# Kernel optimization log

Hardware: AMD Instinct MI355X
Metric: run time of the kernel (lower is better)

Reference implementation:

```python
import jax, jax.numpy as jnp
import numpy as np

B, S = 1, 2048
D = 2048            # n_embd
H = 16              # num heads
KV = 4              # num kv heads
GROUPS = H // KV
D_NOPE = 128
D_ROPE = 64
D_QK = D_NOPE + D_ROPE   # 192
D_V = 128
Q_RANK = 1536
KV_RANK = 512
EPS = 1e-6
MAX_POS = 4096


def rms_norm(x, w, eps=EPS):
    x32 = x.astype(jnp.float32)
    y = x32 * jax.lax.rsqrt(jnp.mean(x32 * x32, axis=-1, keepdims=True) + eps)
    return y.astype(x.dtype) * w


def rotate_half(x):
    x1, x2 = jnp.split(x, 2, axis=-1)
    return jnp.concatenate((-x2, x1), axis=-1)


def setup_inputs() -> dict:
    key = jax.random.key(0)
    ks = jax.random.split(key, 10)
    inv_freq = 1.0 / (10000.0 ** (jnp.arange(0, D_ROPE, 2, dtype=jnp.float32) / D_ROPE))
    t = jnp.arange(MAX_POS, dtype=jnp.float32)
    freqs = jnp.outer(t, inv_freq)                      # [MAX_POS, D_ROPE//2]
    emb = jnp.concatenate((freqs, freqs), axis=-1)      # [MAX_POS, D_ROPE]
    def lin(k, fan_in, fan_out):
        return jax.random.normal(k, (fan_in, fan_out), dtype=jnp.float32) * (fan_in ** -0.5)
    return {
        "hidden_states": jax.random.normal(ks[0], (B, S, D), dtype=jnp.float32),
        "cos": jnp.cos(emb)[None],                      # [1, MAX_POS, D_ROPE]
        "sin": jnp.sin(emb)[None],
        "wq_a": lin(ks[1], D, Q_RANK),
        "q_a_ln_w": jnp.ones((Q_RANK,), jnp.float32),
        "wq_b": lin(ks[2], Q_RANK, H * D_QK),
        "wkv_a": lin(ks[3], D, KV_RANK + D_ROPE),
        "kv_a_ln_w": jnp.ones((KV_RANK,), jnp.float32),
        "wkv_b": lin(ks[4], KV_RANK, KV * (D_NOPE + D_V)),
        "wo": lin(ks[5], H * D_V, D),
        "cache_position": jnp.arange(S, dtype=jnp.int64),
    }


def reference(hidden_states, cos, sin, wq_a, q_a_ln_w, wq_b, wkv_a, kv_a_ln_w,
              wkv_b, wo, cache_position):
    b, s, _ = hidden_states.shape
    # --- query low-rank path ---
    q_a = hidden_states @ wq_a                           # [B,S,Q_RANK]
    q = rms_norm(q_a, q_a_ln_w) @ wq_b                   # [B,S,H*D_QK]
    q = q.reshape(b, s, H, D_QK).transpose(0, 2, 1, 3)   # [B,H,S,D_QK]
    q_pass, q_rot = q[..., :D_NOPE], q[..., D_NOPE:]
    # --- kv low-rank path ---
    ckv = hidden_states @ wkv_a                          # [B,S,KV_RANK+D_ROPE]
    k_pass_a, k_rot_a = ckv[..., :KV_RANK], ckv[..., KV_RANK:]
    kv = rms_norm(k_pass_a, kv_a_ln_w) @ wkv_b           # [B,S,KV*(D_NOPE+D_V)]
    kv = kv.reshape(b, s, KV, D_NOPE + D_V).transpose(0, 2, 1, 3)  # [B,KV,S,*]
    k_pass, v = kv[..., :D_NOPE], kv[..., D_NOPE:]
    # --- partial RoPE ---
    c = cos[0][cache_position][None, None]               # [1,1,S,D_ROPE]
    sn = sin[0][cache_position][None, None]
    q_rot = q_rot * c + rotate_half(q_rot) * sn          # [B,H,S,D_ROPE]
    k_rot = k_rot_a[:, None]                             # [B,1,S,D_ROPE]
    k_rot = k_rot * c + rotate_half(k_rot) * sn
    k_rot = jnp.broadcast_to(k_rot, (b, KV, s, D_ROPE))
    k = jnp.concatenate((k_pass, k_rot), axis=-1)        # [B,KV,S,D_QK]
    # GQA expansion (repeat_interleave over head dim)
    k = jnp.repeat(k, GROUPS, axis=1)                    # [B,H,S,D_QK]
    v = jnp.repeat(v, GROUPS, axis=1)                    # [B,H,S,D_V]
    q_full = jnp.concatenate((q_pass, q_rot), axis=-1)   # [B,H,S,D_QK]
    # causal SDPA (default scale = 1/sqrt(D_QK), matching torch sdpa)
    scale = 1.0 / jnp.sqrt(jnp.float32(D_QK))
    scores = jnp.einsum("bhqd,bhkd->bhqk", q_full, k) * scale
    causal = jnp.tril(jnp.ones((s, s), dtype=bool))
    scores = jnp.where(causal[None, None], scores, jnp.finfo(scores.dtype).min)
    attn = jax.nn.softmax(scores, axis=-1)
    out = jnp.einsum("bhqk,bhkd->bhqd", attn, v)         # [B,H,S,D_V]
    out = out.transpose(0, 2, 1, 3).reshape(b, s, H * D_V)
    return out @ wo                                      # [B,S,D]
```

## Files before the change

### kernel.cpp

```cpp
#include <hip/hip_runtime.h>
#include <hip/hip_bf16.h>


#define S_LEN 2048
#define D_MODEL 2048
#define NH 16
#define NKV 4
#define D_QK 192
#define D_NOPE 128
#define D_ROPE 64
#define D_V 128
#define Q_RANK 1536
#define KV_RANK 512
#define CKV_PITCH 640
#define QDIM (NH * D_QK)
#define KVDIM (NKV * (D_NOPE + D_V))
#define ODIM (NH * D_V)
#define SCALE_QK 0.07216878364870322f
#define SPLIT 4

#define DT_B16 0
#define DT_F32 1
#define DT_AUTO 2

typedef __bf16 bf16x8 __attribute__((ext_vector_type(8)));
typedef float  f32x4  __attribute__((ext_vector_type(4)));
typedef unsigned short u16x8 __attribute__((ext_vector_type(8)));

typedef __attribute__((address_space(1))) const unsigned int as1_u32;
typedef __attribute__((address_space(3))) unsigned int as3_u32;

__device__ __forceinline__ void gl2lds16(const unsigned short* g, unsigned short* l) {
    __builtin_amdgcn_global_load_lds((as1_u32*)g, (as3_u32*)l, 16, 0, 0);
}

__device__ __forceinline__ float b2f(unsigned short u) {
    return __uint_as_float(((unsigned int)u) << 16);
}
__device__ __forceinline__ unsigned short f2b(float f) {
    unsigned int u = __float_as_uint(f);
    return (unsigned short)((u + 0x7fffu + ((u >> 16) & 1u)) >> 16);
}
__device__ __forceinline__ bool flag_f32(const unsigned* dt) {
    return dt[0] == 0x3F800000u;
}
__device__ __forceinline__ bool eff_f32(int mode, bool f32) {
    return mode == DT_F32 || (mode == DT_AUTO && f32);
}
__device__ __forceinline__ float ldany(const void* p, size_t i, bool f32) {
    return f32 ? ((const float*)p)[i] : b2f(((const unsigned short*)p)[i]);
}

#if __has_builtin(__builtin_amdgcn_mov_dpp)
#define ROR16F(x, n) __int_as_float(__builtin_amdgcn_mov_dpp(__float_as_int(x), 0x120 + (n), 0xf, 0xf, true))
#else
#define ROR16F(x, n) __shfl_xor((x), (n))
#endif

__global__ void __launch_bounds__(256)
cvt_bf16(const void* __restrict__ src, unsigned short* __restrict__ dst,
         int nelem, const unsigned* __restrict__ dt)
{
    const bool f32 = flag_f32(dt);
    for (int i = blockIdx.x * 256 + threadIdx.x; i < nelem; i += gridDim.x * 256)
        dst[i] = f2b(ldany(src, i, f32));
}

__global__ void __launch_bounds__(256)
transpose_w(const void* __restrict__ W, int Kdim, int Ncols,
            unsigned short* __restrict__ WT, const unsigned* __restrict__ dt)
{
    __shared__ unsigned short tile[64][65];
    const bool f32 = flag_f32(dt);
    const int k0 = blockIdx.x * 64, n0 = blockIdx.y * 64;
    const int t = threadIdx.x;

    for (int i = t; i < 4096; i += 256) {
        int r = i >> 6, c = i & 63;
        float v = (n0 + c < Ncols) ? ldany(W, (size_t)(k0 + r) * Ncols + n0 + c, f32) : 0.f;
        tile[c][r] = f2b(v);
    }
    __syncthreads();
    for (int i = t; i < 4096; i += 256) {
        int nn = i >> 6, kk = i & 63;
        WT[(size_t)(n0 + nn) * Kdim + k0 + kk] = tile[nn][kk];
    }
}

__global__ void __launch_bounds__(256)
gemm_mfma(const unsigned short* __restrict__ A, int lda,
          const unsigned short* __restrict__ BT, int ldb,
          void* __restrict__ C, int ldc, int K, int cm,
          const unsigned* __restrict__ dt,
          void* __restrict__ C2, int ldc2, int ncol1)
{
    __shared__ unsigned short As[2][128 * 32];
    __shared__ unsigned short Bs[2][128 * 32];

    const int t = threadIdx.x;
    const int w = t >> 6, lane = t & 63;
    const int wr = w & 1, wc = w >> 1;
    const int n = lane & 15, quad = lane >> 4;
    const int row0 = blockIdx.y << 7;
    int col0 = blockIdx.x << 7;
    const int e0 = (w * 64 + lane) * 8;
    const int e1 = e0 + 2048;

    f32x4 acc[4][4];
#pragma unroll
    for (int i = 0; i < 4; ++i)
#pragma unroll
        for (int j = 0; j < 4; ++j) acc[i][j] = (f32x4){0.f, 0.f, 0.f, 0.f};

    gl2lds16(A  + (size_t)(row0 + (e0 >> 5)) * lda + (e0 & 31), &As[0][e0]);
    gl2lds16(A  + (size_t)(row0 + (e1 >> 5)) * lda + (e1 & 31), &As[0][e1]);
    gl2lds16(BT + (size_t)(col0 + (e0 >> 5)) * ldb + (e0 & 31), &Bs[0][e0]);
    gl2lds16(BT + (size_t)(col0 + (e1 >> 5)) * ldb + (e1 & 31), &Bs[0][e1]);

    int cur = 0;
    for (int k0 = 0; k0 < K; k0 += 32) {
        __syncthreads();

        if (k0 + 32 < K) {
            const int kn = k0 + 32;
            gl2lds16(A  + (size_t)(row0 + (e0 >> 5)) * lda + kn + (e0 & 31), &As[cur ^ 1][e0]);
            gl2lds16(A  + (size_t)(row0 + (e1 >> 5)) * lda + kn + (e1 & 31), &As[cur ^ 1][e1]);
            gl2lds16(BT + (size_t)(col0 + (e0 >> 5)) * ldb + kn + (e0 & 31), &Bs[cur ^ 1][e0]);
            gl2lds16(BT + (size_t)(col0 + (e1 >> 5)) * ldb + kn + (e1 & 31), &Bs[cur ^ 1][e1]);
        }

        bf16x8 af[4], bfr[4];
#pragma unroll
        for (int i = 0; i < 4; ++i)
            af[i] = *(const bf16x8*)&As[cur][(wr * 64 + i * 16 + n) * 32 + quad * 8];
#pragma unroll
        for (int j = 0; j < 4; ++j)
            bfr[j] = *(const bf16x8*)&Bs[cur][(wc * 64 + j * 16 + n) * 32 + quad * 8];
#pragma unroll
        for (int i = 0; i < 4; ++i)
#pragma unroll
            for (int j = 0; j < 4; ++j)
                acc[i][j] = __builtin_amdgcn_mfma_f32_16x16x32_bf16(af[i], bfr[j], acc[i][j], 0, 0, 0);

        cur ^= 1;
    }

    void* Cp = C; int ld = ldc;
    if (col0 >= ncol1) { Cp = C2; ld = ldc2; col0 -= ncol1; }

    const bool cf = eff_f32(cm, flag_f32(dt));
#pragma unroll
    for (int i = 0; i < 4; ++i)
#pragma unroll
        for (int r = 0; r < 4; ++r) {
            const int row = row0 + wr * 64 + i * 16 + quad * 4 + r;
            if (cf) {
                float* crow = (float*)Cp + (size_t)row * ld + col0 + wc * 64 + n;
#pragma unroll
                for (int j = 0; j < 4; ++j) crow[j * 16] = acc[i][j][r];
            } else {
                unsigned short* crow = (unsigned short*)Cp + (size_t)row * ld + col0 + wc * 64 + n;
#pragma unroll
                for (int j = 0; j < 4; ++j) crow[j * 16] = f2b(acc[i][j][r]);
            }
        }
}

__global__ void __launch_bounds__(256)
rmsnorm_b(unsigned short* __restrict__ buf, int pitch, int ncols,
          const void* __restrict__ w, const unsigned* __restrict__ dt)
{
    const bool f32 = flag_f32(dt);
    const int row = blockIdx.x;
    const int t = threadIdx.x;
    unsigned short* x = buf + (size_t)row * pitch;

    float ss = 0.f;
    for (int i = t; i < ncols; i += 256) { float v = b2f(x[i]); ss += v * v; }
#pragma unroll
    for (int o = 32; o > 0; o >>= 1) ss += __shfl_down(ss, o);

    __shared__ float part[4];
    __shared__ float sc;
    if ((t & 63) == 0) part[t >> 6] = ss;
    __syncthreads();
    if (t == 0) {
        float tot = part[0] + part[1] + part[2] + part[3];
        sc = rsqrtf(tot / (float)ncols + 1e-6f);
    }
    __syncthreads();
    float scale = sc;
    for (int i = t; i < ncols; i += 256)
        x[i] = f2b(b2f(x[i]) * scale * ldany(w, i, f32));
}

__global__ void __launch_bounds__(256)
rope_k(unsigned short* __restrict__ q, unsigned short* __restrict__ ckvb,
       const void* __restrict__ cosb, const void* __restrict__ sinb,
       const void* __restrict__ cpos, const unsigned* __restrict__ dt)
{
    const bool f32 = flag_f32(dt);
    const int s = blockIdx.x;
    const int t = threadIdx.x;
    const long long* p64 = (const long long*)cpos;
    const int* p32 = (const int*)cpos;
    const bool is64 = (p64[1] == 1LL);
    const int pos = is64 ? (int)p64[s] : p32[s];
    const size_t cb = (size_t)pos * D_ROPE;

    for (int idx = t; idx < NH * 32; idx += 256) {
        int h = idx >> 5, i = idx & 31;
        unsigned short* base = q + (size_t)s * QDIM + h * D_QK + D_NOPE;
        float x1 = b2f(base[i]), x2 = b2f(base[i + 32]);
        float c1 = ldany(cosb, cb + i, f32),      s1 = ldany(sinb, cb + i, f32);
        float c2 = ldany(cosb, cb + i + 32, f32), s2 = ldany(sinb, cb + i + 32, f32);
        base[i]      = f2b(x1 * c1 - x2 * s1);
        base[i + 32] = f2b(x2 * c2 + x1 * s2);
    }
    if (t < 32) {
        int i = t;
        unsigned short* base = ckvb + (size_t)s * CKV_PITCH + KV_RANK;
        float x1 = b2f(base[i]), x2 = b2f(base[i + 32]);
        float c1 = ldany(cosb, cb + i, f32),      s1 = ldany(sinb, cb + i, f32);
        float c2 = ldany(cosb, cb + i + 32, f32), s2 = ldany(sinb, cb + i + 32, f32);
        base[i]      = f2b(x1 * c1 - x2 * s1);
        base[i + 32] = f2b(x2 * c2 + x1 * s2);
    }
}

__global__ void __launch_bounds__(256)
transpose_v(const unsigned short* __restrict__ kvb, unsigned short* __restrict__ vt)
{
    __shared__ unsigned short tile[64][68];
    const int kb = blockIdx.x;
    const int kvh = blockIdx.y >> 1;
    const int d0 = (blockIdx.y & 1) * 64;
    const int t = threadIdx.x;

    for (int i = t; i < 64 * 16; i += 256) {
        int r = i >> 4, c4 = (i & 15) << 2;
        ushort4 v = *(const ushort4*)(kvb + (size_t)(kb * 64 + r) * KVDIM
                                      + kvh * 256 + D_NOPE + d0 + c4);
        tile[c4 + 0][r] = v.x;
        tile[c4 + 1][r] = v.y;
        tile[c4 + 2][r] = v.z;
        tile[c4 + 3][r] = v.w;
    }
    __syncthreads();
    for (int i = t; i < 64 * 16; i += 256) {
        int d = i >> 4, k4 = (i & 15) << 2;
        ushort4 v = *(const ushort4*)&tile[d][k4];
        *(ushort4*)(vt + (size_t)(kvh * 128 + d0 + d) * S_LEN + kb * 64 + k4) = v;
    }
}

__global__ void __launch_bounds__(256, 2)
attn_mfma(const unsigned short* __restrict__ q, const unsigned short* __restrict__ kvb,
          const unsigned short* __restrict__ ckvb, const unsigned short* __restrict__ vt,
          unsigned short* __restrict__ pO, float* __restrict__ pm, float* __restrict__ pl)
{
    const int h   = blockIdx.y;
    const int qtb = (int)gridDim.x - 1 - (int)blockIdx.x;
    const int sp  = blockIdx.z;
    const int kvh = h >> 2;
    const int jtmax = 2 * qtb + 1;

    __shared__ unsigned short ks[64][200];
    __shared__ unsigned short vs[128][72];
    __shared__ unsigned short ps[4][2][16][72];

    const int t = threadIdx.x;
    const int w = t >> 6, lane = t & 63;
    const int n = lane & 15, quad = lane >> 4;
    const int qrow0 = qtb * 128 + w * 16;

    bf16x8 qf[2][6];
#pragma unroll
    for (int g = 0; g < 2; ++g) {
        const unsigned short* qrow = q + (size_t)(qrow0 + g * 64 + n) * QDIM + h * D_QK;
#pragma unroll
        for (int s = 0; s < 6; ++s)
            qf[g][s] = *(const bf16x8*)(qrow + s * 32 + quad * 8);
    }

    f32x4 o[2][8];
#pragma unroll
    for (int g = 0; g < 2; ++g)
#pragma unroll
        for (int c = 0; c < 8; ++c) o[g][c] = (f32x4){0.f, 0.f, 0.f, 0.f};
    float mrow[2][4], lrow[2][4];
#pragma unroll
    for (int g = 0; g < 2; ++g)
#pragma unroll
        for (int i = 0; i < 4; ++i) { mrow[g][i] = -3e38f; lrow[g][i] = 0.f; }

    u16x8 kn[4], kr[2], vv[4];

#define PRELOAD(K0)                                                            \
    {                                                                          \
        const int k0_ = (K0);                                                  \
        _Pragma("unroll")                                                      \
        for (int i = 0; i < 4; ++i) {                                          \
            int g = i * 256 + t, r = g >> 4, c = g & 15;                       \
            kn[i] = *(const u16x8*)(kvb + (size_t)(k0_ + r) * KVDIM            \
                                    + kvh * 256 + c * 8);                      \
        }                                                                      \
        _Pragma("unroll")                                                      \
        for (int i = 0; i < 2; ++i) {                                          \
            int g = i * 256 + t, r = g >> 3, c = g & 7;                        \
            kr[i] = *(const u16x8*)(ckvb + (size_t)(k0_ + r) * CKV_PITCH       \
                                    + KV_RANK + c * 8);                        \
        }                                                                      \
        _Pragma("unroll")                                                      \
        for (int i = 0; i < 4; ++i) {                                          \
            int g = i * 256 + t, d = g >> 3, c = g & 7;                        \
            vv[i] = *(const u16x8*)(vt + (size_t)(kvh * 128 + d) * S_LEN       \
                                    + k0_ + c * 8);                            \
        }                                                                      \
    }

    if (sp <= jtmax) PRELOAD(sp << 6);

    for (int jt = sp; jt <= jtmax; jt += SPLIT) {
        __syncthreads();
#pragma unroll
        for (int i = 0; i < 4; ++i) {
            int g = i * 256 + t, r = g >> 4, c = g & 15;
            *(u16x8*)&ks[r][c * 8] = kn[i];
        }
#pragma unroll
        for (int i = 0; i < 2; ++i) {
            int g = i * 256 + t, r = g >> 3, c = g & 7;
            *(u16x8*)&ks[r][128 + c * 8] = kr[i];
        }
#pragma unroll
        for (int i = 0; i < 4; ++i) {
            int g = i * 256 + t, d = g >> 3, c = g & 7;
            *(u16x8*)&vs[d][c * 8] = vv[i];
        }
        __syncthreads();

        if (jt + SPLIT <= jtmax) PRELOAD((jt + SPLIT) << 6);

        const bool act0  = (jt <= 2 * qtb);
        const bool diag0 = (jt == 2 * qtb);
        const bool diag1 = (jt == jtmax);

        f32x4 sf[2][4];
        __builtin_amdgcn_s_setprio(1);
#pragma unroll
        for (int f = 0; f < 4; ++f) {
            f32x4 a0 = (f32x4){0.f, 0.f, 0.f, 0.f};
            f32x4 a1 = (f32x4){0.f, 0.f, 0.f, 0.f};
#pragma unroll
            for (int s = 0; s < 6; ++s) {
                bf16x8 kf = *(const bf16x8*)&ks[f * 16 + n][s * 32 + quad * 8];
                a0 = __builtin_amdgcn_mfma_f32_16x16x32_bf16(qf[0][s], kf, a0, 0, 0, 0);
                a1 = __builtin_amdgcn_mfma_f32_16x16x32_bf16(qf[1][s], kf, a1, 0, 0, 0);
            }
            sf[0][f] = a0; sf[1][f] = a1;
        }
        __builtin_amdgcn_s_setprio(0);

        const bool actg[2]  = {act0, true};
        const bool diagg[2] = {diag0, diag1};

#pragma unroll
        for (int g = 0; g < 2; ++g) {
            if (!actg[g]) continue;
            const bool dg = diagg[g];
#pragma unroll
            for (int f = 0; f < 4; ++f)
#pragma unroll
                for (int i = 0; i < 4; ++i) {
                    float v = sf[g][f][i] * SCALE_QK;
                    if (dg && (f * 16 + n > w * 16 + quad * 4 + i)) v = -3e38f;
                    sf[g][f][i] = v;
                }

            float lmax[4], fac[4], alpha[4], lsum[4];
#pragma unroll
            for (int i = 0; i < 4; ++i)
                lmax[i] = fmaxf(fmaxf(fmaxf(sf[g][0][i], sf[g][1][i]),
                                      fmaxf(sf[g][2][i], sf[g][3][i])), mrow[g][i]);
#pragma unroll
            for (int f = 0; f < 4; ++f)
#pragma unroll
                for (int i = 0; i < 4; ++i)
                    sf[g][f][i] = __expf(sf[g][f][i] - lmax[i]);
#pragma unroll
            for (int i = 0; i < 4; ++i) {
                lsum[i] = (sf[g][0][i] + sf[g][1][i]) + (sf[g][2][i] + sf[g][3][i]);
                float gm = lmax[i];
                gm = fmaxf(gm, ROR16F(gm, 8));
                gm = fmaxf(gm, ROR16F(gm, 4));
                gm = fmaxf(gm, ROR16F(gm, 2));
                gm = fmaxf(gm, ROR16F(gm, 1));
                fac[i]   = __expf(lmax[i] - gm);
                alpha[i] = __expf(mrow[g][i] - gm);
                mrow[g][i] = gm;
                float s = lsum[i] * fac[i];
                s += ROR16F(s, 8);
                s += ROR16F(s, 4);
                s += ROR16F(s, 2);
                s += ROR16F(s, 1);
                lrow[g][i] = lrow[g][i] * alpha[i] + s;
#pragma unroll
                for (int c = 0; c < 8; ++c) o[g][c][i] *= alpha[i];
            }
#pragma unroll
            for (int f = 0; f < 4; ++f)
#pragma unroll
                for (int i = 0; i < 4; ++i)
                    ps[w][g][quad * 4 + i][f * 16 + n] = f2b(sf[g][f][i] * fac[i]);
        }

        __asm__ __volatile__("s_waitcnt lgkmcnt(0)" ::: "memory");

        bf16x8 pa[2][2];
#pragma unroll
        for (int g = 0; g < 2; ++g) {
            if (actg[g]) {
                pa[g][0] = *(const bf16x8*)&ps[w][g][n][quad * 8];
                pa[g][1] = *(const bf16x8*)&ps[w][g][n][32 + quad * 8];
            } else {
                pa[g][0] = (bf16x8)(__bf16)0.f;
                pa[g][1] = (bf16x8)(__bf16)0.f;
            }
        }

        __builtin_amdgcn_s_setprio(1);
#pragma unroll
        for (int c = 0; c < 8; ++c) {
            bf16x8 v0 = *(const bf16x8*)&vs[c * 16 + n][quad * 8];
            bf16x8 v1 = *(const bf16x8*)&vs[c * 16 + n][32 + quad * 8];
            o[0][c] = __builtin_amdgcn_mfma_f32_16x16x32_bf16(pa[0][0], v0, o[0][c], 0, 0, 0);
            o[0][c] = __builtin_amdgcn_mfma_f32_16x16x32_bf16(pa[0][1], v1, o[0][c], 0, 0, 0);
            o[1][c] = __builtin_amdgcn_mfma_f32_16x16x32_bf16(pa[1][0], v0, o[1][c], 0, 0, 0);
            o[1][c] = __builtin_amdgcn_mfma_f32_16x16x32_bf16(pa[1][1], v1, o[1][c], 0, 0, 0);
        }
        __builtin_amdgcn_s_setprio(0);
    }
#undef PRELOAD

#pragma unroll
    for (int g = 0; g < 2; ++g)
#pragma unroll
        for (int i = 0; i < 4; ++i) {
            const int row = qrow0 + g * 64 + quad * 4 + i;
            const size_t slot = ((size_t)(sp * S_LEN + row) * NH + h);
            unsigned short* orow = pO + slot * 128 + n;
#pragma unroll
            for (int c = 0; c < 8; ++c)
                orow[c * 16] = f2b(o[g][c][i]);
            if (n == 0) { pm[slot] = mrow[g][i]; pl[slot] = lrow[g][i]; }
        }
}

__global__ void __launch_bounds__(256)
combine_k(const unsigned short* __restrict__ pO, const float* __restrict__ pm,
          const float* __restrict__ pl, unsigned short* __restrict__ obuf)
{
    const int row = blockIdx.x;
    const int t = threadIdx.x;
    __shared__ float wsc[NH][SPLIT];

    if (t < NH) {
        const int h = t;
        float m[SPLIT], l[SPLIT];
        float mx = -3e38f;
#pragma unroll
        for (int s = 0; s < SPLIT; ++s) {
            const size_t slot = ((size_t)(s * S_LEN + row) * NH + h);
            m[s] = pm[slot]; l[s] = pl[slot];
            mx = fmaxf(mx, m[s]);
        }
        float lsum = 0.f;
#pragma unroll
        for (int s = 0; s < SPLIT; ++s) lsum += __expf(m[s] - mx) * l[s];
        float inv = 1.f / lsum;
#pragma unroll
        for (int s = 0; s < SPLIT; ++s) wsc[h][s] = __expf(m[s] - mx) * inv;
    }
    __syncthreads();

    for (int idx = t; idx < ODIM; idx += 256) {
        const int h = idx >> 7, d = idx & 127;
        float sum = 0.f;
#pragma unroll
        for (int s = 0; s < SPLIT; ++s) {
            const size_t slot = ((size_t)(s * S_LEN + row) * NH + h);
            sum += b2f(pO[slot * 128 + d]) * wsc[h][s];
        }
        obuf[(size_t)row * ODIM + idx] = f2b(sum);
    }
}


extern "C" void kernel_launch(void* const* d_in, const int* in_sizes, int n_in,
                              void* d_out, int out_size, void* d_ws, size_t ws_size,
                              hipStream_t stream)
{
    const void* hs    = d_in[0];
    const void* cosb  = d_in[1];
    const void* sinb  = d_in[2];
    const void* wq_a  = d_in[3];
    const void* q_ln  = d_in[4];
    const void* wq_b  = d_in[5];
    const void* wkv_a = d_in[6];
    const void* kv_ln = d_in[7];
    const void* wkv_b = d_in[8];
    const void* wo    = d_in[9];
    const void* cpos  = d_in[10];
    const unsigned* dt = (const unsigned*)d_in[4];

    char* ws = (char*)d_ws;
    unsigned short* woT   = (unsigned short*)ws; ws += (size_t)D_MODEL * ODIM    * 2;
    unsigned short* ckvb  = (unsigned short*)ws; ws += (size_t)S_LEN * CKV_PITCH * 2;
    unsigned short* qbuf  = (unsigned short*)ws; ws += (size_t)S_LEN * QDIM      * 2;
    unsigned short* kvb   = (unsigned short*)ws; ws += (size_t)S_LEN * KVDIM     * 2;
    unsigned short* vtb   = (unsigned short*)ws; ws += (size_t)NKV * D_V * S_LEN * 2;
    unsigned short* obuf  = (unsigned short*)ws; ws += (size_t)S_LEN * ODIM      * 2;

    char* scratch = ws;
    unsigned short* hsb   = (unsigned short*)scratch;
    unsigned short* wqaT  = hsb   + (size_t)S_LEN * D_MODEL;
    unsigned short* wkvaT = wqaT  + (size_t)Q_RANK * D_MODEL;
    unsigned short* wqbT  = wkvaT + (size_t)CKV_PITCH * D_MODEL;
    unsigned short* wkvbT = wqbT  + (size_t)QDIM * Q_RANK;
    unsigned short* q_a   = wkvbT + (size_t)KVDIM * KV_RANK;
    unsigned short* pO    = (unsigned short*)scratch;
    float*          pm    = (float*)(pO + (size_t)SPLIT * S_LEN * NH * 128);
    float*          pl    = pm + (size_t)SPLIT * S_LEN * NH;

    cvt_bf16<<<1024, 256, 0, stream>>>(hs, hsb, S_LEN * D_MODEL, dt);
    transpose_w<<<dim3(D_MODEL / 64, Q_RANK / 64), 256, 0, stream>>>(wq_a, D_MODEL, Q_RANK, wqaT, dt);
    transpose_w<<<dim3(D_MODEL / 64, CKV_PITCH / 64), 256, 0, stream>>>(wkv_a, D_MODEL, KV_RANK + D_ROPE, wkvaT, dt);
    transpose_w<<<dim3(Q_RANK / 64, QDIM / 64), 256, 0, stream>>>(wq_b, Q_RANK, QDIM, wqbT, dt);
    transpose_w<<<dim3(KV_RANK / 64, KVDIM / 64), 256, 0, stream>>>(wkv_b, KV_RANK, KVDIM, wkvbT, dt);
    transpose_w<<<dim3(D_MODEL / 64, D_MODEL / 64), 256, 0, stream>>>(wo, ODIM, D_MODEL, woT, dt);

    gemm_mfma<<<dim3((Q_RANK + CKV_PITCH) / 128, S_LEN / 128), 256, 0, stream>>>(
        hsb, D_MODEL, wqaT, D_MODEL, q_a, Q_RANK, D_MODEL, DT_B16, dt,
        ckvb, CKV_PITCH, Q_RANK);

    rmsnorm_b<<<S_LEN, 256, 0, stream>>>(q_a, Q_RANK, Q_RANK, q_ln, dt);
    rmsnorm_b<<<S_LEN, 256, 0, stream>>>(ckvb, CKV_PITCH, KV_RANK, kv_ln, dt);

    gemm_mfma<<<dim3(QDIM / 128, S_LEN / 128), 256, 0, stream>>>(
        q_a, Q_RANK, wqbT, Q_RANK, qbuf, QDIM, Q_RANK, DT_B16, dt,
        nullptr, 0, 1 << 30);
    gemm_mfma<<<dim3(KVDIM / 128, S_LEN / 128), 256, 0, stream>>>(
        ckvb, CKV_PITCH, wkvbT, KV_RANK, kvb, KVDIM, KV_RANK, DT_B16, dt,
        nullptr, 0, 1 << 30);

    rope_k<<<S_LEN, 256, 0, stream>>>(qbuf, ckvb, cosb, sinb, cpos, dt);

    transpose_v<<<dim3(S_LEN / 64, 8), 256, 0, stream>>>(kvb, vtb);

    attn_mfma<<<dim3(S_LEN / 128, NH, SPLIT), 256, 0, stream>>>(
        qbuf, kvb, ckvb, vtb, pO, pm, pl);
    combine_k<<<S_LEN, 256, 0, stream>>>(pO, pm, pl, obuf);

    gemm_mfma<<<dim3(D_MODEL / 128, S_LEN / 128), 256, 0, stream>>>(
        obuf, ODIM, woT, D_MODEL, d_out, D_MODEL, D_MODEL, DT_AUTO, dt,
        nullptr, 0, 1 << 30);
}
```

Measured before the change: 416.5 us.

## Split GEMM K-loop across two wave groups with LDS reduction

```diff
diff --git a/kernel.cpp b/kernel.cpp
--- a/kernel.cpp
+++ b/kernel.cpp
@@ -87,24 +87,25 @@
     }
 }
 
-__global__ void __launch_bounds__(256)
+__global__ void __launch_bounds__(512)
 gemm_mfma(const unsigned short* __restrict__ A, int lda,
           const unsigned short* __restrict__ BT, int ldb,
           void* __restrict__ C, int ldc, int K, int cm,
           const unsigned* __restrict__ dt,
           void* __restrict__ C2, int ldc2, int ncol1)
 {
-    __shared__ unsigned short As[2][128 * 32];
-    __shared__ unsigned short Bs[2][128 * 32];
+    __shared__ unsigned short smem[2][2][2][4096];
 
     const int t = threadIdx.x;
     const int w = t >> 6, lane = t & 63;
-    const int wr = w & 1, wc = w >> 1;
+    const int half = w >> 2;
+    const int wq = w & 3;
+    const int wr = wq & 1, wc = wq >> 1;
     const int n = lane & 15, quad = lane >> 4;
     const int row0 = blockIdx.y << 7;
     int col0 = blockIdx.x << 7;
-    const int e0 = (w * 64 + lane) * 8;
-    const int e1 = e0 + 2048;
+    const int e0 = t * 8;
+    const int er = e0 >> 5, ec = e0 & 31;
 
     f32x4 acc[4][4];
 #pragma unroll
@@ -112,30 +113,36 @@
 #pragma unroll
         for (int j = 0; j < 4; ++j) acc[i][j] = (f32x4){0.f, 0.f, 0.f, 0.f};
 
-    gl2lds16(A  + (size_t)(row0 + (e0 >> 5)) * lda + (e0 & 31), &As[0][e0]);
-    gl2lds16(A  + (size_t)(row0 + (e1 >> 5)) * lda + (e1 & 31), &As[0][e1]);
-    gl2lds16(BT + (size_t)(col0 + (e0 >> 5)) * ldb + (e0 & 31), &Bs[0][e0]);
-    gl2lds16(BT + (size_t)(col0 + (e1 >> 5)) * ldb + (e1 & 31), &Bs[0][e1]);
+#define STAGE(BUF, KB)                                                         \
+    do {                                                                       \
+        gl2lds16(A  + (size_t)(row0 + er) * lda + (KB) + ec,                   \
+                 &smem[BUF][0][0][e0]);                                        \
+        gl2lds16(A  + (size_t)(row0 + er) * lda + (KB) + 32 + ec,              \
+                 &smem[BUF][0][1][e0]);                                        \
+        gl2lds16(BT + (size_t)(col0 + er) * ldb + (KB) + ec,                   \
+                 &smem[BUF][1][0][e0]);                                        \
+        gl2lds16(BT + (size_t)(col0 + er) * ldb + (KB) + 32 + ec,              \
+                 &smem[BUF][1][1][e0]);                                        \
+    } while (0)
+
+    STAGE(0, 0);
 
     int cur = 0;
-    for (int k0 = 0; k0 < K; k0 += 32) {
+    for (int k0 = 0; k0 < K; k0 += 64) {
         __syncthreads();
 
-        if (k0 + 32 < K) {
-            const int kn = k0 + 32;
-            gl2lds16(A  + (size_t)(row0 + (e0 >> 5)) * lda + kn + (e0 & 31), &As[cur ^ 1][e0]);
-            gl2lds16(A  + (size_t)(row0 + (e1 >> 5)) * lda + kn + (e1 & 31), &As[cur ^ 1][e1]);
-            gl2lds16(BT + (size_t)(col0 + (e0 >> 5)) * ldb + kn + (e0 & 31), &Bs[cur ^ 1][e0]);
-            gl2lds16(BT + (size_t)(col0 + (e1 >> 5)) * ldb + kn + (e1 & 31), &Bs[cur ^ 1][e1]);
-        }
+        if (k0 + 64 < K) STAGE(cur ^ 1, k0 + 64);
+
+        const unsigned short* Asub = &smem[cur][0][half][0];
+        const unsigned short* Bsub = &smem[cur][1][half][0];
 
         bf16x8 af[4], bfr[4];
 #pragma unroll
         for (int i = 0; i < 4; ++i)
-            af[i] = *(const bf16x8*)&As[cur][(wr * 64 + i * 16 + n) * 32 + quad * 8];
+            af[i] = *(const bf16x8*)&Asub[(wr * 64 + i * 16 + n) * 32 + quad * 8];
 #pragma unroll
         for (int j = 0; j < 4; ++j)
-            bfr[j] = *(const bf16x8*)&Bs[cur][(wc * 64 + j * 16 + n) * 32 + quad * 8];
+            bfr[j] = *(const bf16x8*)&Bsub[(wc * 64 + j * 16 + n) * 32 + quad * 8];
 #pragma unroll
         for (int i = 0; i < 4; ++i)
 #pragma unroll
@@ -144,26 +151,51 @@
 
         cur ^= 1;
     }
-
-    void* Cp = C; int ld = ldc;
-    if (col0 >= ncol1) { Cp = C2; ld = ldc2; col0 -= ncol1; }
-
-    const bool cf = eff_f32(cm, flag_f32(dt));
-#pragma unroll
-    for (int i = 0; i < 4; ++i)
-#pragma unroll
-        for (int r = 0; r < 4; ++r) {
-            const int row = row0 + wr * 64 + i * 16 + quad * 4 + r;
-            if (cf) {
-                float* crow = (float*)Cp + (size_t)row * ld + col0 + wc * 64 + n;
-#pragma unroll
-                for (int j = 0; j < 4; ++j) crow[j * 16] = acc[i][j][r];
-            } else {
-                unsigned short* crow = (unsigned short*)Cp + (size_t)row * ld + col0 + wc * 64 + n;
-#pragma unroll
-                for (int j = 0; j < 4; ++j) crow[j * 16] = f2b(acc[i][j][r]);
+#undef STAGE
+
+    __syncthreads();
+    float* fsm = (float*)smem;
+    if (half == 1) {
+        float* dst = fsm + wq * 4096;
+#pragma unroll
+        for (int i = 0; i < 4; ++i)
+#pragma unroll
+            for (int j = 0; j < 4; ++j)
+#pragma unroll
+                for (int r = 0; r < 4; ++r)
+                    dst[(i * 16 + quad * 4 + r) * 64 + j * 16 + n] = acc[i][j][r];
+    }
+    __syncthreads();
+    if (half == 0) {
+        const float* src = fsm + wq * 4096;
+#pragma unroll
+        for (int i = 0; i < 4; ++i)
+#pragma unroll
+            for (int j = 0; j < 4; ++j)
+#pragma unroll
+                for (int r = 0; r < 4; ++r)
+                    acc[i][j][r] += src[(i * 16 + quad * 4 + r) * 64 + j * 16 + n];
+
+        void* Cp = C; int ld = ldc;
+        if (col0 >= ncol1) { Cp = C2; ld = ldc2; col0 -= ncol1; }
+
+        const bool cf = eff_f32(cm, flag_f32(dt));
+#pragma unroll
+        for (int i = 0; i < 4; ++i)
+#pragma unroll
+            for (int r = 0; r < 4; ++r) {
+                const int row = row0 + wr * 64 + i * 16 + quad * 4 + r;
+                if (cf) {
+                    float* crow = (float*)Cp + (size_t)row * ld + col0 + wc * 64 + n;
+#pragma unroll
+                    for (int j = 0; j < 4; ++j) crow[j * 16] = acc[i][j][r];
+                } else {
+                    unsigned short* crow = (unsigned short*)Cp + (size_t)row * ld + col0 + wc * 64 + n;
+#pragma unroll
+                    for (int j = 0; j < 4; ++j) crow[j * 16] = f2b(acc[i][j][r]);
+                }
             }
-        }
+    }
 }
 
 __global__ void __launch_bounds__(256)
@@ -540,17 +572,17 @@
     transpose_w<<<dim3(KV_RANK / 64, KVDIM / 64), 256, 0, stream>>>(wkv_b, KV_RANK, KVDIM, wkvbT, dt);
     transpose_w<<<dim3(D_MODEL / 64, D_MODEL / 64), 256, 0, stream>>>(wo, ODIM, D_MODEL, woT, dt);
 
-    gemm_mfma<<<dim3((Q_RANK + CKV_PITCH) / 128, S_LEN / 128), 256, 0, stream>>>(
+    gemm_mfma<<<dim3((Q_RANK + CKV_PITCH) / 128, S_LEN / 128), 512, 0, stream>>>(
         hsb, D_MODEL, wqaT, D_MODEL, q_a, Q_RANK, D_MODEL, DT_B16, dt,
         ckvb, CKV_PITCH, Q_RANK);
 
     rmsnorm_b<<<S_LEN, 256, 0, stream>>>(q_a, Q_RANK, Q_RANK, q_ln, dt);
     rmsnorm_b<<<S_LEN, 256, 0, stream>>>(ckvb, CKV_PITCH, KV_RANK, kv_ln, dt);
 
-    gemm_mfma<<<dim3(QDIM / 128, S_LEN / 128), 256, 0, stream>>>(
+    gemm_mfma<<<dim3(QDIM / 128, S_LEN / 128), 512, 0, stream>>>(
         q_a, Q_RANK, wqbT, Q_RANK, qbuf, QDIM, Q_RANK, DT_B16, dt,
         nullptr, 0, 1 << 30);
-    gemm_mfma<<<dim3(KVDIM / 128, S_LEN / 128), 256, 0, stream>>>(
+    gemm_mfma<<<dim3(KVDIM / 128, S_LEN / 128), 512, 0, stream>>>(
         ckvb, CKV_PITCH, wkvbT, KV_RANK, kvb, KVDIM, KV_RANK, DT_B16, dt,
         nullptr, 0, 1 << 30);
 
@@ -562,7 +594,7 @@
         qbuf, kvb, ckvb, vtb, pO, pm, pl);
     combine_k<<<S_LEN, 256, 0, stream>>>(pO, pm, pl, obuf);
 
-    gemm_mfma<<<dim3(D_MODEL / 128, S_LEN / 128), 256, 0, stream>>>(
+    gemm_mfma<<<dim3(D_MODEL / 128, S_LEN / 128), 512, 0, stream>>>(
         obuf, ODIM, woT, D_MODEL, d_out, D_MODEL, D_MODEL, DT_AUTO, dt,
         nullptr, 0, 1 << 30);
 }
```

Result: faster. 403.7 us (-3.1%).
